# Kernel optimization log

Measured on AMD Instinct MI355X. Metric: run time of the kernel, lower is better.

## Reference

```python
import jax, jax.numpy as jnp
import numpy as np

EMBED_DIM = 128
CANCER_DIM = 32
N_NODES = 50000
N_EDGES = 800000
INPUT_DIM = EMBED_DIM * 2 + CANCER_DIM + 3  # 291
HIDDEN_DIM = INPUT_DIM // 2  # 145


def setup_inputs() -> dict:
    key = jax.random.key(0)
    ks = jax.random.split(key, 8)
    h = jax.random.normal(ks[0], (N_NODES, EMBED_DIM), dtype=jnp.float32)
    edge_index = jax.random.randint(ks[1], (2, N_EDGES), 0, N_NODES, dtype=jnp.int64)
    cancer_embedding = jax.random.normal(ks[2], (1, CANCER_DIM), dtype=jnp.float32)
    causal_scores = jax.random.uniform(ks[3], (N_NODES, 1), dtype=jnp.float32)
    # MLP params (Linear stores weight [out, in]; we keep [in, out] for x @ W)
    lim1 = 1.0 / np.sqrt(INPUT_DIM)
    W1 = jax.random.uniform(ks[4], (INPUT_DIM, HIDDEN_DIM), minval=-lim1, maxval=lim1, dtype=jnp.float32)
    b1 = jax.random.uniform(ks[5], (HIDDEN_DIM,), minval=-lim1, maxval=lim1, dtype=jnp.float32)
    lim2 = 1.0 / np.sqrt(HIDDEN_DIM)
    W2 = jax.random.uniform(ks[6], (HIDDEN_DIM, 1), minval=-lim2, maxval=lim2, dtype=jnp.float32)
    b2 = jax.random.uniform(ks[7], (1,), minval=-lim2, maxval=lim2, dtype=jnp.float32)
    return {"h": h, "edge_index": edge_index, "cancer_embedding": cancer_embedding,
            "causal_scores": causal_scores, "W1": W1, "b1": b1, "W2": W2, "b2": b2}


def reference(h, edge_index, cancer_embedding, causal_scores, W1, b1, W2, b2):
    src, dst = edge_index[0], edge_index[1]
    h_i = h[src]                         # [E, D]
    h_j = h[dst]                         # [E, D]
    c_i = causal_scores[src]             # [E, 1]
    c_j = causal_scores[dst]             # [E, 1]
    causal_diff = c_i - c_j              # [E, 1]
    num_edges = edge_index.shape[1]
    cancer_exp = jnp.broadcast_to(cancer_embedding, (num_edges, cancer_embedding.shape[-1]))
    edge_features = jnp.concatenate([h_i, h_j, cancer_exp, c_i, c_j, causal_diff], axis=-1)  # [E, INPUT_DIM]
    hid = jax.nn.relu(edge_features @ W1 + b1)          # [E, HIDDEN]
    out = jax.nn.sigmoid(hid @ W2 + b2)                 # [E, 1]
    return out.squeeze(-1)                              # [E]
```

## Files before the change

kernel.cpp:

```cpp
#include <hip/hip_runtime.h>
#include <hip/hip_bf16.h>
#include <stdint.h>

#define EMBED 128
#define HID 145
#define HSTR 160
#define NTILE 20
#define KCH 4
#define MROWB 128
#define LROW 152
#define HB2ROW 272

typedef __attribute__((ext_vector_type(8))) short short8;
typedef __attribute__((ext_vector_type(4))) float f32x4;

__device__ __forceinline__ uint16_t f2bf(float f) {
    uint32_t x = __float_as_uint(f);
    x += 0x7FFFu + ((x >> 16) & 1u);
    return (uint16_t)(x >> 16);
}
__device__ __forceinline__ short f2bf_cvt(float f) {
    union { __bf16 h; short s; } u_;
    u_.h = (__bf16)f;
    return u_.s;
}

__global__ void __launch_bounds__(256)
prep_fused(const float* __restrict__ cancer, const float* __restrict__ W1,
           const float* __restrict__ b1, const float* __restrict__ W2,
           const void* __restrict__ eiv, int E, int P,
           float* __restrict__ b1p, float* __restrict__ wci,
           float* __restrict__ wcj, float* __restrict__ w2p,
           short* __restrict__ Wpb, uint32_t* __restrict__ pairs)
{
    const int t = threadIdx.x;
    const int b = blockIdx.x;
    if (b < P) {
        const uint32_t* pw = (const uint32_t*)eiv;
        const uint32_t odd = pw[1] | pw[3] | pw[5] | pw[7] | pw[9] | pw[11] | pw[13] | pw[15];
        const int is64 = (odd == 0u);
        const int e = b * 256 + t;
        if (e < E) {
            uint32_t src, dst;
            if (is64) {
                const long long* e64 = (const long long*)eiv;
                src = (uint32_t)e64[e]; dst = (uint32_t)e64[(size_t)E + e];
            } else {
                const uint32_t* e32 = (const uint32_t*)eiv;
                src = e32[e];           dst = e32[(size_t)E + e];
            }
            pairs[e] = (src << 16) | (dst & 0xFFFFu);
        }
        return;
    }
    if (b < P + 160) {
        const int idx = (b - P) * 256 + t;
        const int reg  = idx & 7;
        const int lane = (idx >> 3) & 63;
        const int tl   = idx >> 9;
        const int tt   = tl % NTILE;
        const int kc   = tl / NTILE;
        const int k    = kc * 32 + (lane >> 4) * 8 + reg;
        const int col  = tt * 16 + (lane & 15);
        float val = 0.f;
        if (col < HID)                             val = W1[(size_t)k * HID + col];
        else if (col >= HSTR && col < HSTR + HID)  val = W1[(size_t)(EMBED + k) * HID + (col - HSTR)];
        Wpb[idx] = (short)f2bf(val);
        return;
    }
    if (t < HSTR) {
        float bv = 0.f, a = 0.f, bb = 0.f, w2 = 0.f;
        if (t < HID) {
            float s = b1[t];
            #pragma unroll
            for (int k = 0; k < 32; ++k)
                s = fmaf(cancer[k], W1[(size_t)(2 * EMBED + k) * HID + t], s);
            bv = s;
            a  = W1[(size_t)288 * HID + t] + W1[(size_t)290 * HID + t];
            bb = W1[(size_t)289 * HID + t] - W1[(size_t)290 * HID + t];
            w2 = W2[t];
        }
        b1p[t] = bv; wci[t] = a; wcj[t] = bb; w2p[t] = w2;
    }
}

__global__ void __launch_bounds__(256)
proj_mfma(const float* __restrict__ h, const short* __restrict__ Wpb,
          const float* __restrict__ causal, const float* __restrict__ b1p,
          const float* __restrict__ wci, const float* __restrict__ wcj,
          uint8_t* __restrict__ u, uint8_t* __restrict__ v, int nNodes)
{
    __shared__ __align__(16) uint8_t smem[2 * 64 * LROW];
    __shared__ float pmax[2][2][64];

    const int t = threadIdx.x;
    const int lane = t & 63;
    const int w = t >> 6;
    const int lane15 = lane & 15, hi = lane >> 4;
    const int n0blk = blockIdx.x * 64;
    const bool full = (n0blk + 64 <= nNodes);

    const float4* hsrc = (const float4*)(h + (size_t)n0blk * EMBED);
    if (full) {
        #pragma unroll
        for (int k = 0; k < 8; ++k) {
            const int f = k * 256 + t;
            const float4 x = hsrc[f];
            const uint32_t lo = (uint32_t)(uint16_t)f2bf_cvt(x.x)
                              | ((uint32_t)(uint16_t)f2bf_cvt(x.y) << 16);
            const uint32_t hg = (uint32_t)(uint16_t)f2bf_cvt(x.z)
                              | ((uint32_t)(uint16_t)f2bf_cvt(x.w) << 16);
            *(uint2*)(smem + (f >> 5) * HB2ROW + (f & 31) * 8) = make_uint2(lo, hg);
        }
    } else {
        #pragma unroll
        for (int k = 0; k < 8; ++k) {
            const int f = k * 256 + t;
            const int row = f >> 5;
            float4 x = make_float4(0.f, 0.f, 0.f, 0.f);
            if (n0blk + row < nNodes) x = hsrc[f];
            const uint32_t lo = (uint32_t)(uint16_t)f2bf_cvt(x.x)
                              | ((uint32_t)(uint16_t)f2bf_cvt(x.y) << 16);
            const uint32_t hg = (uint32_t)(uint16_t)f2bf_cvt(x.z)
                              | ((uint32_t)(uint16_t)f2bf_cvt(x.w) << 16);
            *(uint2*)(smem + row * HB2ROW + (f & 31) * 8) = make_uint2(lo, hg);
        }
    }
    __syncthreads();

    const int w5 = 5 * w;
    const uint8_t* habase = smem + lane15 * HB2ROW + hi * 16;

    f32x4 acc[4][5];
    #pragma unroll
    for (int g = 0; g < 4; ++g)
        #pragma unroll
        for (int i = 0; i < 5; ++i) acc[g][i] = (f32x4){0.f, 0.f, 0.f, 0.f};

    const short8* bp = (const short8*)Wpb;
    #pragma unroll
    for (int kc = 0; kc < KCH; ++kc) {
        short8 bfr[5];
        #pragma unroll
        for (int i = 0; i < 5; ++i)
            bfr[i] = bp[(kc * NTILE + w5 + i) * 64 + lane];
        #pragma unroll
        for (int g = 0; g < 4; ++g) {
            const short8 a = *(const short8*)(habase + g * 16 * HB2ROW + kc * 64);
            #pragma unroll
            for (int i = 0; i < 5; ++i)
                acc[g][i] = __builtin_amdgcn_mfma_f32_16x16x32_bf16(a, bfr[i], acc[g][i], 0, 0, 0);
        }
    }

    const int tb = w >> 1, hf = w & 1;
    float addB[5], addC[5];
    #pragma unroll
    for (int i = 0; i < 5; ++i) {
        const int col = (w5 + i) * 16 + lane15;
        const int ccol = tb ? col - HSTR : col;
        addB[i] = tb ? 0.f : b1p[ccol];
        addC[i] = tb ? wcj[ccol] : wci[ccol];
    }
    #pragma unroll
    for (int g = 0; g < 4; ++g) {
        float cz[4];
        #pragma unroll
        for (int j = 0; j < 4; ++j) {
            const int n = n0blk + g * 16 + hi * 4 + j;
            cz[j] = (n < nNodes) ? causal[n] : 0.f;
        }
        #pragma unroll
        for (int i = 0; i < 5; ++i)
            #pragma unroll
            for (int j = 0; j < 4; ++j)
                acc[g][i][j] += fmaf(cz[j], addC[i], addB[i]);
    }

    #pragma unroll
    for (int g = 0; g < 4; ++g) {
        #pragma unroll
        for (int j = 0; j < 4; ++j) {
            float m = fmaxf(fmaxf(fmaxf(fabsf(acc[g][0][j]), fabsf(acc[g][1][j])),
                                  fmaxf(fabsf(acc[g][2][j]), fabsf(acc[g][3][j]))),
                            fabsf(acc[g][4][j]));
            #pragma unroll
            for (int mk = 1; mk < 16; mk <<= 1) m = fmaxf(m, __shfl_xor(m, mk));
            if (lane15 == 0) pmax[tb][hf][g * 16 + hi * 4 + j] = m;
        }
    }
    __syncthreads();

    uint8_t* ldsu = smem;
    uint8_t* ldsv = smem + 64 * LROW;
    uint8_t* myt = tb ? ldsv : ldsu;
    #pragma unroll
    for (int g = 0; g < 4; ++g) {
        #pragma unroll
        for (int j = 0; j < 4; ++j) {
            const int row = g * 16 + hi * 4 + j;
            const float mm = fmaxf(fmaxf(pmax[tb][0][row], pmax[tb][1][row]), 1e-20f);
            const float inv = 31.f / mm;
            if (hf == 0 && lane15 == 0)
                *(float*)(myt + row * LROW + 148) = mm * (1.f / 31.f);
            #pragma unroll
            for (int i = 0; i < 5; ++i) {
                const int ccol = (w5 + i) * 16 + lane15 - (tb ? HSTR : 0);
                const uint8_t q = (uint8_t)(uint32_t)(acc[g][i][j] * inv + 32.5f);
                if (ccol < 145)
                    myt[row * LROW + ccol] = q;
            }
        }
    }
    __syncthreads();

    char* ug = (char*)u + (size_t)n0blk * MROWB;
    char* vg = (char*)v + (size_t)n0blk * MROWB;
    #pragma unroll
    for (int i = 0; i < 2; ++i) {
        const int idx = i * 256 + t;
        const int row = idx >> 3, c = idx & 7;
        if (!full && n0blk + row >= nNodes) continue;
        #pragma unroll
        for (int tab = 0; tab < 2; ++tab) {
            const uint8_t* lr = (tab ? ldsv : ldsu) + row * LROW;
            uint4 o;
            if (c < 7) {
                const uint32_t* wp = (const uint32_t*)(lr + 20 * c);
                const uint32_t b0 = wp[0], b1_ = wp[1], b2 = wp[2], b3 = wp[3], b4 = wp[4];
                o.x = (b0 & 63u) | (((b0 >> 8) & 63u) << 6) | (((b0 >> 16) & 63u) << 12)
                    | (((b0 >> 24) & 63u) << 18) | ((b1_ & 63u) << 24);
                o.y = ((b1_ >> 8) & 63u) | (((b1_ >> 16) & 63u) << 6) | (((b1_ >> 24) & 63u) << 12)
                    | ((b2 & 63u) << 18) | (((b2 >> 8) & 63u) << 24);
                o.z = ((b2 >> 16) & 63u) | (((b2 >> 24) & 63u) << 6) | ((b3 & 63u) << 12)
                    | (((b3 >> 8) & 63u) << 18) | (((b3 >> 16) & 63u) << 24);
                o.w = ((b3 >> 24) & 63u) | ((b4 & 63u) << 6) | (((b4 >> 8) & 63u) << 12)
                    | (((b4 >> 16) & 63u) << 18) | (((b4 >> 24) & 63u) << 24);
            } else {
                const uint32_t w0 = *(const uint32_t*)(lr + 140);
                const uint32_t w1 = *(const uint32_t*)(lr + 144);
                o.x = (w0 & 63u) | (((w0 >> 8) & 63u) << 6) | (((w0 >> 16) & 63u) << 12)
                    | (((w0 >> 24) & 63u) << 18) | ((w1 & 63u) << 24);
                o.y = *(const uint32_t*)(lr + 148);
                o.z = 0u; o.w = 0u;
            }
            *(uint4*)((tab ? vg : ug) + 16 * idx) = o;
        }
    }
}

__global__ void __launch_bounds__(256)
edge_int6(const uint32_t* __restrict__ pairs,
          const uint8_t* __restrict__ u, const uint8_t* __restrict__ v,
          const float* __restrict__ w2p, const float* __restrict__ b2,
          float* __restrict__ out, int E)
{
    const int t = threadIdx.x;
    const int lane = t & 63;
    const int r = lane & 3;
    const int grp = lane >> 2;
    const int wid = blockIdx.x * (blockDim.x >> 6) + (t >> 6);
    const int base = wid * 32;
    const int e0 = base + grp, e1 = base + 16 + grp;
    const bool ok0 = e0 < E, ok1 = e1 < E;
    const float bias2 = *b2;

    const uint32_t pr0 = pairs[ok0 ? e0 : 0];
    const uint32_t pr1 = pairs[ok1 ? e1 : 0];

    const uint4* ua = (const uint4*)(u + (pr0 >> 16)     * (uint32_t)MROWB) + 2 * r;
    const uint4* va = (const uint4*)(v + (pr0 & 0xFFFFu) * (uint32_t)MROWB) + 2 * r;
    const uint4* ub = (const uint4*)(u + (pr1 >> 16)     * (uint32_t)MROWB) + 2 * r;
    const uint4* vb = (const uint4*)(v + (pr1 & 0xFFFFu) * (uint32_t)MROWB) + 2 * r;
    const uint4 UA0 = ua[0], UA1 = ua[1];
    const uint4 VA0 = va[0], VA1 = va[1];
    const uint4 UB0 = ub[0], UB1 = ub[1];
    const uint4 VB0 = vb[0], VB1 = vb[1];

    const int l3 = lane | 3;
    const float su0 = __shfl(__uint_as_float(UA1.y), l3);
    const float sv0 = __shfl(__uint_as_float(VA1.y), l3);
    const float su1 = __shfl(__uint_as_float(UB1.y), l3);
    const float sv1 = __shfl(__uint_as_float(VB1.y), l3);
    const float off0 = -32.f * (su0 + sv0);
    const float off1 = -32.f * (su1 + sv1);

    uint32_t uw0[8] = {UA0.x, UA0.y, UA0.z, UA0.w, UA1.x, UA1.y, UA1.z, UA1.w};
    uint32_t vw0[8] = {VA0.x, VA0.y, VA0.z, VA0.w, VA1.x, VA1.y, VA1.z, VA1.w};
    uint32_t uw1[8] = {UB0.x, UB0.y, UB0.z, UB0.w, UB1.x, UB1.y, UB1.z, UB1.w};
    uint32_t vw1[8] = {VB0.x, VB0.y, VB0.z, VB0.w, VB1.x, VB1.y, VB1.z, VB1.w};

    const float* w2b = w2p + 40 * r;
    float acc0 = 0.f, acc1 = 0.f;
    #pragma unroll
    for (int lw = 0; lw < 8; ++lw) {
        #pragma unroll
        for (int k = 0; k < 5; ++k) {
            const float w2v = w2b[5 * lw + k];
            const float uf0 = (float)((uw0[lw] >> (6 * k)) & 63u);
            const float vf0 = (float)((vw0[lw] >> (6 * k)) & 63u);
            float tv0 = fmaf(su0, uf0, fmaf(sv0, vf0, off0));
            tv0 = fmaxf(tv0, 0.f);
            acc0 = fmaf(tv0, w2v, acc0);
            const float uf1 = (float)((uw1[lw] >> (6 * k)) & 63u);
            const float vf1 = (float)((vw1[lw] >> (6 * k)) & 63u);
            float tv1 = fmaf(su1, uf1, fmaf(sv1, vf1, off1));
            tv1 = fmaxf(tv1, 0.f);
            acc1 = fmaf(tv1, w2v, acc1);
        }
    }
    acc0 += __shfl_xor(acc0, 1);
    acc0 += __shfl_xor(acc0, 2);
    acc1 += __shfl_xor(acc1, 1);
    acc1 += __shfl_xor(acc1, 2);
    if (r == 0 && ok0) out[e0] = 1.f / (1.f + __expf(-(acc0 + bias2)));
    if (r == 0 && ok1) out[e1] = 1.f / (1.f + __expf(-(acc1 + bias2)));
}

__global__ void __launch_bounds__(256)
fallback_kernel(const void* __restrict__ eiv, const float* __restrict__ h,
                const float* __restrict__ cancer, const float* __restrict__ causal,
                const float* __restrict__ W1, const float* __restrict__ b1,
                const float* __restrict__ W2, const float* __restrict__ b2,
                float* __restrict__ out, int E)
{
    const int lane = threadIdx.x & 63;
    const int wpb  = blockDim.x >> 6;
    const int wid  = blockIdx.x * wpb + (threadIdx.x >> 6);
    const int nW   = gridDim.x * wpb;
    const uint32_t* p32 = (const uint32_t*)eiv;
    const uint32_t o = p32[1] | p32[3] | p32[5] | p32[7] | p32[9] | p32[11] | p32[13] | p32[15];
    const int is64 = (o == 0u);
    const long long* e64 = (const long long*)eiv;
    const int*       e32 = (const int*)eiv;
    const float bias2 = *b2;

    for (int e = wid; e < E; e += nW) {
        long long src, dst;
        if (is64) { src = e64[e]; dst = e64[(size_t)E + e]; }
        else      { src = e32[e]; dst = e32[(size_t)E + e]; }
        const float ci = causal[src], cj = causal[dst];
        float acc0 = 0.f, acc1 = 0.f, acc2 = 0.f;
        const int j0 = lane, j1 = lane + 64, j2 = lane + 128;
        for (int k = 0; k < 291; ++k) {
            float f;
            if      (k < 128) f = h[(size_t)src * 128 + k];
            else if (k < 256) f = h[(size_t)dst * 128 + (k - 128)];
            else if (k < 288) f = cancer[k - 256];
            else if (k == 288) f = ci;
            else if (k == 289) f = cj;
            else               f = ci - cj;
            const float* wr = W1 + (size_t)k * HID;
            acc0 = fmaf(f, wr[j0], acc0);
            acc1 = fmaf(f, wr[j1], acc1);
            if (j2 < HID) acc2 = fmaf(f, wr[j2], acc2);
        }
        float partial = fmaxf(acc0 + b1[j0], 0.f) * W2[j0]
                      + fmaxf(acc1 + b1[j1], 0.f) * W2[j1];
        if (j2 < HID) partial += fmaxf(acc2 + b1[j2], 0.f) * W2[j2];
        #pragma unroll
        for (int m = 32; m; m >>= 1) partial += __shfl_xor(partial, m, 64);
        if (lane == 0) out[e] = 1.f / (1.f + __expf(-(partial + bias2)));
    }
}

extern "C" void kernel_launch(void* const* d_in, const int* in_sizes, int n_in,
                              void* d_out, int out_size, void* d_ws, size_t ws_size,
                              hipStream_t stream)
{
    const float* h      = (const float*)d_in[0];
    const void*  ei     = d_in[1];
    const float* cancer = (const float*)d_in[2];
    const float* causal = (const float*)d_in[3];
    const float* W1     = (const float*)d_in[4];
    const float* b1     = (const float*)d_in[5];
    const float* W2     = (const float*)d_in[6];
    const float* b2     = (const float*)d_in[7];
    float* outp = (float*)d_out;

    const int nNodes = in_sizes[0] / EMBED;
    const int E      = in_sizes[1] / 2;

    const size_t WPB_OFF   = 8192;
    const size_t PAIRS_OFF = 98304;
    const size_t pairsB    = ((size_t)E * 4 + 255) & ~(size_t)255;
    const size_t tabB      = (size_t)nNodes * MROWB;
    const size_t U_OFF     = PAIRS_OFF + pairsB;
    const size_t V_OFF     = (U_OFF + tabB + 255) & ~(size_t)255;
    const size_t need      = V_OFF + tabB;

    char* ws = (char*)d_ws;
    float* b1p  = (float*)(ws + 1024);
    float* wci  = (float*)(ws + 2048);
    float* wcj  = (float*)(ws + 3072);
    float* w2p  = (float*)(ws + 4096);
    short* Wpb  = (short*)(ws + WPB_OFF);

    if (ws_size >= need && nNodes <= 65536) {
        uint32_t* pairs = (uint32_t*)(ws + PAIRS_OFF);
        uint8_t*  u     = (uint8_t*)(ws + U_OFF);
        uint8_t*  v     = (uint8_t*)(ws + V_OFF);

        const int P = (E + 255) / 256;
        prep_fused<<<P + 161, 256, 0, stream>>>(cancer, W1, b1, W2, ei, E, P,
                                                b1p, wci, wcj, w2p, Wpb, pairs);
        proj_mfma<<<(nNodes + 63) / 64, 256, 0, stream>>>(h, Wpb, causal, b1p,
                                                          wci, wcj, u, v, nNodes);
        const int waves  = (E + 31) / 32;
        const int blocks = (waves + 3) / 4;
        edge_int6<<<blocks, 256, 0, stream>>>(pairs, u, v, w2p, b2, outp, E);
    } else {
        fallback_kernel<<<2048, 256, 0, stream>>>(ei, h, cancer, causal, W1, b1, W2, b2,
                                                  outp, E);
    }
}
```

Measured before the change: 66.59 us.

## Move edge-pair packing into projection kernel and halve projection block rows

The edge-index packing moves out of the prep kernel and into the projection kernel as a grid-stride loop that runs after each block finishes its node tile. The prep kernel shrinks to the 161 weight-preparation blocks. The projection kernel now handles 32 nodes per block instead of 64, doubling the grid to spread the node work over more CUs. The aim is to shorten the small prep launch and overlap the memory-bound pair packing with projection work, at the cost of each block reloading its weight fragments for half as many rows.

New measurement: 67.12 us. About the same (+0.8%).

```diff
diff --git a/kernel.cpp b/kernel.cpp
--- a/kernel.cpp
+++ b/kernel.cpp
@@ -10,6 +10,7 @@
 #define MROWB 128
 #define LROW 152
 #define HB2ROW 272
+#define PBLK 32
 
 typedef __attribute__((ext_vector_type(8))) short short8;
 typedef __attribute__((ext_vector_type(4))) float f32x4;
@@ -28,33 +29,14 @@
 __global__ void __launch_bounds__(256)
 prep_fused(const float* __restrict__ cancer, const float* __restrict__ W1,
            const float* __restrict__ b1, const float* __restrict__ W2,
-           const void* __restrict__ eiv, int E, int P,
            float* __restrict__ b1p, float* __restrict__ wci,
            float* __restrict__ wcj, float* __restrict__ w2p,
-           short* __restrict__ Wpb, uint32_t* __restrict__ pairs)
+           short* __restrict__ Wpb)
 {
     const int t = threadIdx.x;
     const int b = blockIdx.x;
-    if (b < P) {
-        const uint32_t* pw = (const uint32_t*)eiv;
-        const uint32_t odd = pw[1] | pw[3] | pw[5] | pw[7] | pw[9] | pw[11] | pw[13] | pw[15];
-        const int is64 = (odd == 0u);
-        const int e = b * 256 + t;
-        if (e < E) {
-            uint32_t src, dst;
-            if (is64) {
-                const long long* e64 = (const long long*)eiv;
-                src = (uint32_t)e64[e]; dst = (uint32_t)e64[(size_t)E + e];
-            } else {
-                const uint32_t* e32 = (const uint32_t*)eiv;
-                src = e32[e];           dst = e32[(size_t)E + e];
-            }
-            pairs[e] = (src << 16) | (dst & 0xFFFFu);
-        }
-        return;
-    }
-    if (b < P + 160) {
-        const int idx = (b - P) * 256 + t;
+    if (b < 160) {
+        const int idx = b * 256 + t;
         const int reg  = idx & 7;
         const int lane = (idx >> 3) & 63;
         const int tl   = idx >> 9;
@@ -88,52 +70,40 @@
 proj_mfma(const float* __restrict__ h, const short* __restrict__ Wpb,
           const float* __restrict__ causal, const float* __restrict__ b1p,
           const float* __restrict__ wci, const float* __restrict__ wcj,
+          const void* __restrict__ eiv, uint32_t* __restrict__ pairs, int E,
           uint8_t* __restrict__ u, uint8_t* __restrict__ v, int nNodes)
 {
-    __shared__ __align__(16) uint8_t smem[2 * 64 * LROW];
-    __shared__ float pmax[2][2][64];
+    __shared__ __align__(16) uint8_t smem[2 * PBLK * LROW];
+    __shared__ float pmax[2][2][PBLK];
 
     const int t = threadIdx.x;
     const int lane = t & 63;
     const int w = t >> 6;
     const int lane15 = lane & 15, hi = lane >> 4;
-    const int n0blk = blockIdx.x * 64;
-    const bool full = (n0blk + 64 <= nNodes);
+    const int n0blk = blockIdx.x * PBLK;
+    const bool full = (n0blk + PBLK <= nNodes);
 
     const float4* hsrc = (const float4*)(h + (size_t)n0blk * EMBED);
-    if (full) {
-        #pragma unroll
-        for (int k = 0; k < 8; ++k) {
-            const int f = k * 256 + t;
-            const float4 x = hsrc[f];
-            const uint32_t lo = (uint32_t)(uint16_t)f2bf_cvt(x.x)
-                              | ((uint32_t)(uint16_t)f2bf_cvt(x.y) << 16);
-            const uint32_t hg = (uint32_t)(uint16_t)f2bf_cvt(x.z)
-                              | ((uint32_t)(uint16_t)f2bf_cvt(x.w) << 16);
-            *(uint2*)(smem + (f >> 5) * HB2ROW + (f & 31) * 8) = make_uint2(lo, hg);
-        }
-    } else {
-        #pragma unroll
-        for (int k = 0; k < 8; ++k) {
-            const int f = k * 256 + t;
-            const int row = f >> 5;
-            float4 x = make_float4(0.f, 0.f, 0.f, 0.f);
-            if (n0blk + row < nNodes) x = hsrc[f];
-            const uint32_t lo = (uint32_t)(uint16_t)f2bf_cvt(x.x)
-                              | ((uint32_t)(uint16_t)f2bf_cvt(x.y) << 16);
-            const uint32_t hg = (uint32_t)(uint16_t)f2bf_cvt(x.z)
-                              | ((uint32_t)(uint16_t)f2bf_cvt(x.w) << 16);
-            *(uint2*)(smem + row * HB2ROW + (f & 31) * 8) = make_uint2(lo, hg);
-        }
+    #pragma unroll
+    for (int k = 0; k < 4; ++k) {
+        const int f = k * 256 + t;
+        const int row = f >> 5;
+        float4 x = make_float4(0.f, 0.f, 0.f, 0.f);
+        if (full || n0blk + row < nNodes) x = hsrc[f];
+        const uint32_t lo = (uint32_t)(uint16_t)f2bf_cvt(x.x)
+                          | ((uint32_t)(uint16_t)f2bf_cvt(x.y) << 16);
+        const uint32_t hg = (uint32_t)(uint16_t)f2bf_cvt(x.z)
+                          | ((uint32_t)(uint16_t)f2bf_cvt(x.w) << 16);
+        *(uint2*)(smem + row * HB2ROW + (f & 31) * 8) = make_uint2(lo, hg);
     }
     __syncthreads();
 
     const int w5 = 5 * w;
     const uint8_t* habase = smem + lane15 * HB2ROW + hi * 16;
 
-    f32x4 acc[4][5];
-    #pragma unroll
-    for (int g = 0; g < 4; ++g)
+    f32x4 acc[2][5];
+    #pragma unroll
+    for (int g = 0; g < 2; ++g)
         #pragma unroll
         for (int i = 0; i < 5; ++i) acc[g][i] = (f32x4){0.f, 0.f, 0.f, 0.f};
 
@@ -145,7 +115,7 @@
         for (int i = 0; i < 5; ++i)
             bfr[i] = bp[(kc * NTILE + w5 + i) * 64 + lane];
         #pragma unroll
-        for (int g = 0; g < 4; ++g) {
+        for (int g = 0; g < 2; ++g) {
             const short8 a = *(const short8*)(habase + g * 16 * HB2ROW + kc * 64);
             #pragma unroll
             for (int i = 0; i < 5; ++i)
@@ -163,7 +133,7 @@
         addC[i] = tb ? wcj[ccol] : wci[ccol];
     }
     #pragma unroll
-    for (int g = 0; g < 4; ++g) {
+    for (int g = 0; g < 2; ++g) {
         float cz[4];
         #pragma unroll
         for (int j = 0; j < 4; ++j) {
@@ -178,7 +148,7 @@
     }
 
     #pragma unroll
-    for (int g = 0; g < 4; ++g) {
+    for (int g = 0; g < 2; ++g) {
         #pragma unroll
         for (int j = 0; j < 4; ++j) {
             float m = fmaxf(fmaxf(fmaxf(fabsf(acc[g][0][j]), fabsf(acc[g][1][j])),
@@ -192,10 +162,10 @@
     __syncthreads();
 
     uint8_t* ldsu = smem;
-    uint8_t* ldsv = smem + 64 * LROW;
+    uint8_t* ldsv = smem + PBLK * LROW;
     uint8_t* myt = tb ? ldsv : ldsu;
     #pragma unroll
-    for (int g = 0; g < 4; ++g) {
+    for (int g = 0; g < 2; ++g) {
         #pragma unroll
         for (int j = 0; j < 4; ++j) {
             const int row = g * 16 + hi * 4 + j;
@@ -216,36 +186,51 @@
 
     char* ug = (char*)u + (size_t)n0blk * MROWB;
     char* vg = (char*)v + (size_t)n0blk * MROWB;
-    #pragma unroll
-    for (int i = 0; i < 2; ++i) {
-        const int idx = i * 256 + t;
-        const int row = idx >> 3, c = idx & 7;
-        if (!full && n0blk + row >= nNodes) continue;
-        #pragma unroll
-        for (int tab = 0; tab < 2; ++tab) {
-            const uint8_t* lr = (tab ? ldsv : ldsu) + row * LROW;
-            uint4 o;
-            if (c < 7) {
-                const uint32_t* wp = (const uint32_t*)(lr + 20 * c);
-                const uint32_t b0 = wp[0], b1_ = wp[1], b2 = wp[2], b3 = wp[3], b4 = wp[4];
-                o.x = (b0 & 63u) | (((b0 >> 8) & 63u) << 6) | (((b0 >> 16) & 63u) << 12)
-                    | (((b0 >> 24) & 63u) << 18) | ((b1_ & 63u) << 24);
-                o.y = ((b1_ >> 8) & 63u) | (((b1_ >> 16) & 63u) << 6) | (((b1_ >> 24) & 63u) << 12)
-                    | ((b2 & 63u) << 18) | (((b2 >> 8) & 63u) << 24);
-                o.z = ((b2 >> 16) & 63u) | (((b2 >> 24) & 63u) << 6) | ((b3 & 63u) << 12)
-                    | (((b3 >> 8) & 63u) << 18) | (((b3 >> 16) & 63u) << 24);
-                o.w = ((b3 >> 24) & 63u) | ((b4 & 63u) << 6) | (((b4 >> 8) & 63u) << 12)
-                    | (((b4 >> 16) & 63u) << 18) | (((b4 >> 24) & 63u) << 24);
-            } else {
-                const uint32_t w0 = *(const uint32_t*)(lr + 140);
-                const uint32_t w1 = *(const uint32_t*)(lr + 144);
-                o.x = (w0 & 63u) | (((w0 >> 8) & 63u) << 6) | (((w0 >> 16) & 63u) << 12)
-                    | (((w0 >> 24) & 63u) << 18) | ((w1 & 63u) << 24);
-                o.y = *(const uint32_t*)(lr + 148);
-                o.z = 0u; o.w = 0u;
+    {
+        const int row = t >> 3, c = t & 7;
+        if (full || n0blk + row < nNodes) {
+            #pragma unroll
+            for (int tab = 0; tab < 2; ++tab) {
+                const uint8_t* lr = (tab ? ldsv : ldsu) + row * LROW;
+                uint4 o;
+                if (c < 7) {
+                    const uint32_t* wp = (const uint32_t*)(lr + 20 * c);
+                    const uint32_t b0 = wp[0], b1_ = wp[1], b2 = wp[2], b3 = wp[3], b4 = wp[4];
+                    o.x = (b0 & 63u) | (((b0 >> 8) & 63u) << 6) | (((b0 >> 16) & 63u) << 12)
+                        | (((b0 >> 24) & 63u) << 18) | ((b1_ & 63u) << 24);
+                    o.y = ((b1_ >> 8) & 63u) | (((b1_ >> 16) & 63u) << 6) | (((b1_ >> 24) & 63u) << 12)
+                        | ((b2 & 63u) << 18) | (((b2 >> 8) & 63u) << 24);
+                    o.z = ((b2 >> 16) & 63u) | (((b2 >> 24) & 63u) << 6) | ((b3 & 63u) << 12)
+                        | (((b3 >> 8) & 63u) << 18) | (((b3 >> 16) & 63u) << 24);
+                    o.w = ((b3 >> 24) & 63u) | ((b4 & 63u) << 6) | (((b4 >> 8) & 63u) << 12)
+                        | (((b4 >> 16) & 63u) << 18) | (((b4 >> 24) & 63u) << 24);
+                } else {
+                    const uint32_t w0 = *(const uint32_t*)(lr + 140);
+                    const uint32_t w1 = *(const uint32_t*)(lr + 144);
+                    o.x = (w0 & 63u) | (((w0 >> 8) & 63u) << 6) | (((w0 >> 16) & 63u) << 12)
+                        | (((w0 >> 24) & 63u) << 18) | ((w1 & 63u) << 24);
+                    o.y = *(const uint32_t*)(lr + 148);
+                    o.z = 0u; o.w = 0u;
+                }
+                *(uint4*)((tab ? vg : ug) + 16 * t) = o;
             }
-            *(uint4*)((tab ? vg : ug) + 16 * idx) = o;
-        }
+        }
+    }
+
+    const uint32_t* pw = (const uint32_t*)eiv;
+    const uint32_t odd = pw[1] | pw[3] | pw[5] | pw[7] | pw[9] | pw[11] | pw[13] | pw[15];
+    const int is64 = (odd == 0u);
+    const int stride = gridDim.x * 256;
+    for (int e = blockIdx.x * 256 + t; e < E; e += stride) {
+        uint32_t src, dst;
+        if (is64) {
+            const long long* e64 = (const long long*)eiv;
+            src = (uint32_t)e64[e]; dst = (uint32_t)e64[(size_t)E + e];
+        } else {
+            const uint32_t* e32 = (const uint32_t*)eiv;
+            src = e32[e];           dst = e32[(size_t)E + e];
+        }
+        pairs[e] = (src << 16) | (dst & 0xFFFFu);
     }
 }
 
@@ -401,11 +386,10 @@
         uint8_t*  u     = (uint8_t*)(ws + U_OFF);
         uint8_t*  v     = (uint8_t*)(ws + V_OFF);
 
-        const int P = (E + 255) / 256;
-        prep_fused<<<P + 161, 256, 0, stream>>>(cancer, W1, b1, W2, ei, E, P,
-                                                b1p, wci, wcj, w2p, Wpb, pairs);
-        proj_mfma<<<(nNodes + 63) / 64, 256, 0, stream>>>(h, Wpb, causal, b1p,
-                                                          wci, wcj, u, v, nNodes);
+        prep_fused<<<161, 256, 0, stream>>>(cancer, W1, b1, W2,
+                                            b1p, wci, wcj, w2p, Wpb);
+        proj_mfma<<<(nNodes + PBLK - 1) / PBLK, 256, 0, stream>>>(
+            h, Wpb, causal, b1p, wci, wcj, ei, pairs, E, u, v, nNodes);
         const int waves  = (E + 31) / 32;
         const int blocks = (waves + 3) / 4;
         edge_int6<<<blocks, 256, 0, stream>>>(pairs, u, v, w2p, b2, outp, E);
```

## Pack int6 tables directly from MFMA registers and move scales to separate arrays

Applied to the files above, without the earlier changes.

The projection kernel now packs five 6-bit quantized values per 32-bit word straight from the MFMA accumulator layout and writes them to global memory. This drops the LDS staging pass, its extra barrier and the byte-to-int6 repacking. W2 is permuted in the prep kernel to match the new column order. Per-node scales move from inside the table rows into separate uscl/vscl arrays, so the edge kernel makes two extra scalar gathers per edge but no longer needs shuffles. Global writes become scattered 4-byte stores rather than coalesced 16-byte stores, which may cost write efficiency.

Measured after the change: 66.67 us (median of 2 runs). Within noise of the previous version (+0.1%).

```diff
diff --git a/kernel.cpp b/kernel.cpp
--- a/kernel.cpp
+++ b/kernel.cpp
@@ -8,7 +8,6 @@
 #define NTILE 20
 #define KCH 4
 #define MROWB 128
-#define LROW 152
 #define HB2ROW 272
 
 typedef __attribute__((ext_vector_type(8))) short short8;
@@ -30,7 +29,7 @@
            const float* __restrict__ b1, const float* __restrict__ W2,
            const void* __restrict__ eiv, int E, int P,
            float* __restrict__ b1p, float* __restrict__ wci,
-           float* __restrict__ wcj, float* __restrict__ w2p,
+           float* __restrict__ wcj, float* __restrict__ w2q,
            short* __restrict__ Wpb, uint32_t* __restrict__ pairs)
 {
     const int t = threadIdx.x;
@@ -69,7 +68,7 @@
         return;
     }
     if (t < HSTR) {
-        float bv = 0.f, a = 0.f, bb = 0.f, w2 = 0.f;
+        float bv = 0.f, a = 0.f, bb = 0.f;
         if (t < HID) {
             float s = b1[t];
             #pragma unroll
@@ -78,9 +77,12 @@
             bv = s;
             a  = W1[(size_t)288 * HID + t] + W1[(size_t)290 * HID + t];
             bb = W1[(size_t)289 * HID + t] - W1[(size_t)290 * HID + t];
-            w2 = W2[t];
-        }
-        b1p[t] = bv; wci[t] = a; wcj[t] = bb; w2p[t] = w2;
+        }
+        b1p[t] = bv; wci[t] = a; wcj[t] = bb;
+        const int widx = t / 5, i = t % 5;
+        const int hf = widx & 1, l15 = widx >> 1;
+        const int col = (hf * 5 + i) * 16 + l15;
+        w2q[t] = (col < HID) ? W2[col] : 0.f;
     }
 }
 
@@ -88,9 +90,10 @@
 proj_mfma(const float* __restrict__ h, const short* __restrict__ Wpb,
           const float* __restrict__ causal, const float* __restrict__ b1p,
           const float* __restrict__ wci, const float* __restrict__ wcj,
-          uint8_t* __restrict__ u, uint8_t* __restrict__ v, int nNodes)
-{
-    __shared__ __align__(16) uint8_t smem[2 * 64 * LROW];
+          uint8_t* __restrict__ u, uint8_t* __restrict__ v,
+          float* __restrict__ uscl, float* __restrict__ vscl, int nNodes)
+{
+    __shared__ __align__(16) uint8_t smem[64 * HB2ROW];
     __shared__ float pmax[2][2][64];
 
     const int t = threadIdx.x;
@@ -191,60 +194,27 @@
     }
     __syncthreads();
 
-    uint8_t* ldsu = smem;
-    uint8_t* ldsv = smem + 64 * LROW;
-    uint8_t* myt = tb ? ldsv : ldsu;
+    uint32_t* tabw = (uint32_t*)(tb ? v : u);
+    float* sclp = tb ? vscl : uscl;
+    const int widx = lane15 * 2 + hf;
     #pragma unroll
     for (int g = 0; g < 4; ++g) {
         #pragma unroll
         for (int j = 0; j < 4; ++j) {
             const int row = g * 16 + hi * 4 + j;
-            const float mm = fmaxf(fmaxf(pmax[tb][0][row], pmax[tb][1][row]), 1e-20f);
-            const float inv = 31.f / mm;
-            if (hf == 0 && lane15 == 0)
-                *(float*)(myt + row * LROW + 148) = mm * (1.f / 31.f);
-            #pragma unroll
-            for (int i = 0; i < 5; ++i) {
-                const int ccol = (w5 + i) * 16 + lane15 - (tb ? HSTR : 0);
-                const uint8_t q = (uint8_t)(uint32_t)(acc[g][i][j] * inv + 32.5f);
-                if (ccol < 145)
-                    myt[row * LROW + ccol] = q;
+            const int n = n0blk + row;
+            if (full || n < nNodes) {
+                const float mm = fmaxf(fmaxf(pmax[tb][0][row], pmax[tb][1][row]), 1e-20f);
+                const float inv = 31.f / mm;
+                uint32_t wd = 0;
+                #pragma unroll
+                for (int i = 0; i < 5; ++i) {
+                    const uint32_t q = (uint32_t)(acc[g][i][j] * inv + 32.5f) & 63u;
+                    wd |= q << (6 * i);
+                }
+                tabw[(size_t)n * 32 + widx] = wd;
+                if (widx == 0) sclp[n] = mm * (1.f / 31.f);
             }
-        }
-    }
-    __syncthreads();
-
-    char* ug = (char*)u + (size_t)n0blk * MROWB;
-    char* vg = (char*)v + (size_t)n0blk * MROWB;
-    #pragma unroll
-    for (int i = 0; i < 2; ++i) {
-        const int idx = i * 256 + t;
-        const int row = idx >> 3, c = idx & 7;
-        if (!full && n0blk + row >= nNodes) continue;
-        #pragma unroll
-        for (int tab = 0; tab < 2; ++tab) {
-            const uint8_t* lr = (tab ? ldsv : ldsu) + row * LROW;
-            uint4 o;
-            if (c < 7) {
-                const uint32_t* wp = (const uint32_t*)(lr + 20 * c);
-                const uint32_t b0 = wp[0], b1_ = wp[1], b2 = wp[2], b3 = wp[3], b4 = wp[4];
-                o.x = (b0 & 63u) | (((b0 >> 8) & 63u) << 6) | (((b0 >> 16) & 63u) << 12)
-                    | (((b0 >> 24) & 63u) << 18) | ((b1_ & 63u) << 24);
-                o.y = ((b1_ >> 8) & 63u) | (((b1_ >> 16) & 63u) << 6) | (((b1_ >> 24) & 63u) << 12)
-                    | ((b2 & 63u) << 18) | (((b2 >> 8) & 63u) << 24);
-                o.z = ((b2 >> 16) & 63u) | (((b2 >> 24) & 63u) << 6) | ((b3 & 63u) << 12)
-                    | (((b3 >> 8) & 63u) << 18) | (((b3 >> 16) & 63u) << 24);
-                o.w = ((b3 >> 24) & 63u) | ((b4 & 63u) << 6) | (((b4 >> 8) & 63u) << 12)
-                    | (((b4 >> 16) & 63u) << 18) | (((b4 >> 24) & 63u) << 24);
-            } else {
-                const uint32_t w0 = *(const uint32_t*)(lr + 140);
-                const uint32_t w1 = *(const uint32_t*)(lr + 144);
-                o.x = (w0 & 63u) | (((w0 >> 8) & 63u) << 6) | (((w0 >> 16) & 63u) << 12)
-                    | (((w0 >> 24) & 63u) << 18) | ((w1 & 63u) << 24);
-                o.y = *(const uint32_t*)(lr + 148);
-                o.z = 0u; o.w = 0u;
-            }
-            *(uint4*)((tab ? vg : ug) + 16 * idx) = o;
         }
     }
 }
@@ -252,7 +222,8 @@
 __global__ void __launch_bounds__(256)
 edge_int6(const uint32_t* __restrict__ pairs,
           const uint8_t* __restrict__ u, const uint8_t* __restrict__ v,
-          const float* __restrict__ w2p, const float* __restrict__ b2,
+          const float* __restrict__ uscl, const float* __restrict__ vscl,
+          const float* __restrict__ w2q, const float* __restrict__ b2,
           float* __restrict__ out, int E)
 {
     const int t = threadIdx.x;
@@ -267,30 +238,29 @@
 
     const uint32_t pr0 = pairs[ok0 ? e0 : 0];
     const uint32_t pr1 = pairs[ok1 ? e1 : 0];
-
-    const uint4* ua = (const uint4*)(u + (pr0 >> 16)     * (uint32_t)MROWB) + 2 * r;
-    const uint4* va = (const uint4*)(v + (pr0 & 0xFFFFu) * (uint32_t)MROWB) + 2 * r;
-    const uint4* ub = (const uint4*)(u + (pr1 >> 16)     * (uint32_t)MROWB) + 2 * r;
-    const uint4* vb = (const uint4*)(v + (pr1 & 0xFFFFu) * (uint32_t)MROWB) + 2 * r;
+    const uint32_t s0 = pr0 >> 16, d0 = pr0 & 0xFFFFu;
+    const uint32_t s1 = pr1 >> 16, d1 = pr1 & 0xFFFFu;
+
+    const uint4* ua = (const uint4*)(u + s0 * (uint32_t)MROWB) + 2 * r;
+    const uint4* va = (const uint4*)(v + d0 * (uint32_t)MROWB) + 2 * r;
+    const uint4* ub = (const uint4*)(u + s1 * (uint32_t)MROWB) + 2 * r;
+    const uint4* vb = (const uint4*)(v + d1 * (uint32_t)MROWB) + 2 * r;
     const uint4 UA0 = ua[0], UA1 = ua[1];
     const uint4 VA0 = va[0], VA1 = va[1];
     const uint4 UB0 = ub[0], UB1 = ub[1];
     const uint4 VB0 = vb[0], VB1 = vb[1];
 
-    const int l3 = lane | 3;
-    const float su0 = __shfl(__uint_as_float(UA1.y), l3);
-    const float sv0 = __shfl(__uint_as_float(VA1.y), l3);
-    const float su1 = __shfl(__uint_as_float(UB1.y), l3);
-    const float sv1 = __shfl(__uint_as_float(VB1.y), l3);
+    const float su0 = uscl[s0], sv0 = vscl[d0];
+    const float su1 = uscl[s1], sv1 = vscl[d1];
     const float off0 = -32.f * (su0 + sv0);
     const float off1 = -32.f * (su1 + sv1);
 
-    uint32_t uw0[8] = {UA0.x, UA0.y, UA0.z, UA0.w, UA1.x, UA1.y, UA1.z, UA1.w};
-    uint32_t vw0[8] = {VA0.x, VA0.y, VA0.z, VA0.w, VA1.x, VA1.y, VA1.z, VA1.w};
-    uint32_t uw1[8] = {UB0.x, UB0.y, UB0.z, UB0.w, UB1.x, UB1.y, UB1.z, UB1.w};
-    uint32_t vw1[8] = {VB0.x, VB0.y, VB0.z, VB0.w, VB1.x, VB1.y, VB1.z, VB1.w};
-
-    const float* w2b = w2p + 40 * r;
+    const uint32_t uw0[8] = {UA0.x, UA0.y, UA0.z, UA0.w, UA1.x, UA1.y, UA1.z, UA1.w};
+    const uint32_t vw0[8] = {VA0.x, VA0.y, VA0.z, VA0.w, VA1.x, VA1.y, VA1.z, VA1.w};
+    const uint32_t uw1[8] = {UB0.x, UB0.y, UB0.z, UB0.w, UB1.x, UB1.y, UB1.z, UB1.w};
+    const uint32_t vw1[8] = {VB0.x, VB0.y, VB0.z, VB0.w, VB1.x, VB1.y, VB1.z, VB1.w};
+
+    const float* w2b = w2q + 40 * r;
     float acc0 = 0.f, acc1 = 0.f;
     #pragma unroll
     for (int lw = 0; lw < 8; ++lw) {
@@ -384,8 +354,11 @@
     const size_t WPB_OFF   = 8192;
     const size_t PAIRS_OFF = 98304;
     const size_t pairsB    = ((size_t)E * 4 + 255) & ~(size_t)255;
+    const size_t sclB      = ((size_t)nNodes * 4 + 255) & ~(size_t)255;
     const size_t tabB      = (size_t)nNodes * MROWB;
-    const size_t U_OFF     = PAIRS_OFF + pairsB;
+    const size_t USCL_OFF  = PAIRS_OFF + pairsB;
+    const size_t VSCL_OFF  = USCL_OFF + sclB;
+    const size_t U_OFF     = VSCL_OFF + sclB;
     const size_t V_OFF     = (U_OFF + tabB + 255) & ~(size_t)255;
     const size_t need      = V_OFF + tabB;
 
@@ -393,22 +366,26 @@
     float* b1p  = (float*)(ws + 1024);
     float* wci  = (float*)(ws + 2048);
     float* wcj  = (float*)(ws + 3072);
-    float* w2p  = (float*)(ws + 4096);
+    float* w2q  = (float*)(ws + 4096);
     short* Wpb  = (short*)(ws + WPB_OFF);
 
     if (ws_size >= need && nNodes <= 65536) {
         uint32_t* pairs = (uint32_t*)(ws + PAIRS_OFF);
+        float*    uscl  = (float*)(ws + USCL_OFF);
+        float*    vscl  = (float*)(ws + VSCL_OFF);
         uint8_t*  u     = (uint8_t*)(ws + U_OFF);
         uint8_t*  v     = (uint8_t*)(ws + V_OFF);
 
         const int P = (E + 255) / 256;
         prep_fused<<<P + 161, 256, 0, stream>>>(cancer, W1, b1, W2, ei, E, P,
-                                                b1p, wci, wcj, w2p, Wpb, pairs);
+                                                b1p, wci, wcj, w2q, Wpb, pairs);
         proj_mfma<<<(nNodes + 63) / 64, 256, 0, stream>>>(h, Wpb, causal, b1p,
-                                                          wci, wcj, u, v, nNodes);
+                                                          wci, wcj, u, v,
+                                                          uscl, vscl, nNodes);
         const int waves  = (E + 31) / 32;
         const int blocks = (waves + 3) / 4;
-        edge_int6<<<blocks, 256, 0, stream>>>(pairs, u, v, w2p, b2, outp, E);
+        edge_int6<<<blocks, 256, 0, stream>>>(pairs, u, v, uscl, vscl,
+                                              w2q, b2, outp, E);
     } else {
         fallback_kernel<<<2048, 256, 0, stream>>>(ei, h, cancer, causal, W1, b1, W2, b2,
                                                   outp, E);
```
